# Performance work log

Measured on AMD Instinct MI355X. Metric: run time of the kernel, lower is better.

## Reference

```python
import jax, jax.numpy as jnp
import numpy as np

B, T = 1, 2048
N_HEAD = 16
N_KV_HEAD = 16
N_EMBD = 1024
HEAD_DIM = N_EMBD // N_HEAD  # 64
HD8 = HEAD_DIM // 8          # 8 octonion blocks per head
EPS_RMS = 1e-6


def qconj(q):
    return q * jnp.array([1.0, -1.0, -1.0, -1.0], dtype=q.dtype)


def qmul(q1, q2):
    # Hamilton product, (...,4) x (...,4) -> (...,4)
    w1, x1, y1, z1 = (q1[..., 0], q1[..., 1], q1[..., 2], q1[..., 3])
    w2, x2, y2, z2 = (q2[..., 0], q2[..., 1], q2[..., 2], q2[..., 3])
    return jnp.stack([
        w1 * w2 - x1 * x2 - y1 * y2 - z1 * z2,
        w1 * x2 + x1 * w2 + y1 * z2 - z1 * y2,
        w1 * y2 - x1 * z2 + y1 * w2 + z1 * x2,
        w1 * z2 + x1 * y2 - y1 * x2 + z1 * w2,
    ], axis=-1)


def omul(o1, o2):
    # Cayley-Dickson octonion product, (...,8)
    a, b = o1[..., :4], o1[..., 4:]
    c, d = o2[..., :4], o2[..., 4:]
    first = qmul(a, c) - qmul(qconj(d), b)
    second = qmul(d, a) + qmul(b, qconj(c))
    return jnp.concatenate([first, second], axis=-1)


def oconj(o):
    return jnp.concatenate([qconj(o[..., :4]), -o[..., 4:]], axis=-1)


# Octonion multiplication structure constants: omul(x, y)[k] = x[a] y[p] C[a,p,k]
_EYE8 = jnp.eye(8, dtype=jnp.float32)
C_OCT = jax.vmap(lambda ei: jax.vmap(lambda ej: omul(ei, ej))(_EYE8))(_EYE8)  # (8,8,8)
# Trilinear tensor for omul(omul(q, kc), v):  T3[a,p,q,k] = sum_e C[a,p,e] C[e,q,k]
T3 = jnp.einsum('ape,eqk->apqk', C_OCT, C_OCT)  # (8,8,8,8)


def apply_rotary_emb(x, cos, sin):
    # x: (B, T, H, hd); cos/sin: (1, T, 1, hd//2)
    d = x.shape[-1] // 2
    x1, x2 = x[..., :d], x[..., d:]
    y1 = x1 * cos + x2 * sin
    y2 = x2 * cos - x1 * sin
    return jnp.concatenate([y1, y2], axis=-1)


def rms_norm(x):
    return x * jax.lax.rsqrt(jnp.mean(x * x, axis=-1, keepdims=True) + EPS_RMS)


def setup_inputs() -> dict:
    key = jax.random.key(0)
    ks = jax.random.split(key, 7)
    x = jax.random.normal(ks[0], (B, T, N_EMBD), dtype=jnp.float32)
    cos = jax.random.uniform(ks[1], (1, T, 1, HEAD_DIM // 2), dtype=jnp.float32)
    sin = jax.random.uniform(ks[2], (1, T, 1, HEAD_DIM // 2), dtype=jnp.float32)
    s = 0.02
    Wq = jax.random.normal(ks[3], (N_HEAD * HEAD_DIM, N_EMBD), dtype=jnp.float32) * s
    Wk = jax.random.normal(ks[4], (N_KV_HEAD * HEAD_DIM, N_EMBD), dtype=jnp.float32) * s
    Wv = jax.random.normal(ks[5], (N_KV_HEAD * HEAD_DIM, N_EMBD), dtype=jnp.float32) * s
    Wo = jax.random.normal(ks[6], (N_EMBD, N_EMBD), dtype=jnp.float32) * s
    return {"x": x, "cos": cos, "sin": sin, "Wq": Wq, "Wk": Wk, "Wv": Wv, "Wo": Wo}


def reference(x, cos, sin, Wq, Wk, Wv, Wo):
    Bx, Tx, Cx = x.shape
    q = (x @ Wq.T).reshape(Bx, Tx, N_HEAD, HEAD_DIM)
    k = (x @ Wk.T).reshape(Bx, Tx, N_KV_HEAD, HEAD_DIM)
    v = (x @ Wv.T).reshape(Bx, Tx, N_KV_HEAD, HEAD_DIM)
    q = rms_norm(apply_rotary_emb(q, cos, sin))
    k = rms_norm(apply_rotary_emb(k, cos, sin))
    q = q.transpose(0, 2, 1, 3)  # (B,H,T,hd)
    k = k.transpose(0, 2, 1, 3)
    v = v.transpose(0, 2, 1, 3)

    q_o = q.reshape(Bx, N_HEAD, Tx, HD8, 8)
    k_o = k.reshape(Bx, N_KV_HEAD, Tx, HD8, 8)
    v_o = v.reshape(Bx, N_KV_HEAD, Tx, HD8, 8)
    # F.normalize(p=2, dim=-1): divide by max(||.||, 1e-12)
    k_o = k_o / jnp.maximum(jnp.linalg.norm(k_o, axis=-1, keepdims=True), 1e-12)

    # Scores use the (pre-octonion-normalized) rotary+rms k
    scores = jnp.einsum('bhid,bhjd->bhij', q, k) * (HEAD_DIM ** -0.5)
    mask = jnp.tril(jnp.ones((Tx, Tx), dtype=bool))
    scores = jnp.where(mask, scores, -jnp.inf)
    probs = jax.nn.softmax(scores, axis=-1)  # (B,H,Tq,Tk)

    # y_i = sum_j p_ij * omul(omul(q_i, oconj(k_j)), v_j)
    # omul is bilinear, so pull the j-sum inside:
    # y_i[k] = q_i[a] * T3[a,p,c,k] * (sum_j p_ij kc_j[p] v_j[c])
    kc = oconj(k_o)                                              # (B,H,Tk,M,8)
    KV = jnp.einsum('bhjmp,bhjmq->bhjmpq', kc, v_o)              # (B,H,Tk,M,8,8)
    Z = jnp.einsum('bhij,bhjmpq->bhimpq', probs, KV)             # (B,H,Tq,M,8,8)
    y_o = jnp.einsum('bhima,apqk,bhimpq->bhimk', q_o, T3, Z)     # (B,H,Tq,M,8)

    y = y_o.reshape(Bx, N_HEAD, Tx, HEAD_DIM).transpose(0, 2, 1, 3).reshape(Bx, Tx, Cx)
    return y @ Wo.T
```

## Files before the change

kernel.cpp:

```cpp
#include <hip/hip_runtime.h>

typedef unsigned short u16;
typedef unsigned int u32;

#define T_SEQ 2048
#define NHEAD 16
#define HDIM 64
#define CDIM 1024
#define W_HSTR (512*2048)
#define Z_HSTR (2048*512)

#define SGBITS 0xB2D8741EACC66A00ULL

#define EXP2C 0.18033688011112042f

typedef _Float16 f16x8 __attribute__((ext_vector_type(8)));
typedef float f32x4 __attribute__((ext_vector_type(4)));

__device__ __forceinline__ float h2f(u16 u) { _Float16 h; __builtin_memcpy(&h, &u, 2); return (float)h; }
__device__ __forceinline__ u16 f2h(float f) { _Float16 h = (_Float16)f; u16 u; __builtin_memcpy(&u, &h, 2); return u; }
__device__ __forceinline__ u32 pk(float a, float b) { return (u32)f2h(a) | ((u32)f2h(b) << 16); }

__device__ __forceinline__ void gload16(const u16* g, u16* l) {
    __builtin_amdgcn_global_load_lds((const __attribute__((address_space(1))) u32*)g,
                                     (__attribute__((address_space(3))) u32*)l, 16, 0, 0);
}

template<bool F16OUT>
__device__ __forceinline__ void hgemm_tile(const u16* __restrict__ At, int lda,
                                           const u16* __restrict__ Bt, int ldb, int K,
                                           float* __restrict__ Cf, u16* __restrict__ Ch,
                                           int ldc, float scale, u16* As, u16* Bs) {
    int t = threadIdx.x;
    int wave = t >> 6, l = t & 63;
    int wm = wave & 1, wn = wave >> 1;
    int quad = l >> 4, lr = l & 15;
    f32x4 acc[4][4];
#pragma unroll
    for (int i = 0; i < 4; ++i)
#pragma unroll
        for (int j = 0; j < 4; ++j) acc[i][j] = (f32x4){0.f, 0.f, 0.f, 0.f};
    int acol = quad * 8;
    for (int k0 = 0; k0 < K; k0 += 64) {
#pragma unroll
        for (int j = 0; j < 4; ++j) {
            int d = wave * 4 + j;
            int kb = d >> 3, seg = d & 7;
            size_t roff = (size_t)(seg * 16 + lr);
            int coff = k0 + kb * 32 + acol;
            gload16(At + roff * lda + coff, As + d * 512);
            gload16(Bt + roff * ldb + coff, Bs + d * 512);
        }
        __syncthreads();
#pragma unroll
        for (int kb = 0; kb < 2; ++kb) {
            f16x8 af[4], bf[4];
#pragma unroll
            for (int mi = 0; mi < 4; ++mi) af[mi] = *(const f16x8*)&As[(kb * 8 + wm * 4 + mi) * 512 + l * 8];
#pragma unroll
            for (int ni = 0; ni < 4; ++ni) bf[ni] = *(const f16x8*)&Bs[(kb * 8 + wn * 4 + ni) * 512 + l * 8];
#pragma unroll
            for (int mi = 0; mi < 4; ++mi)
#pragma unroll
                for (int ni = 0; ni < 4; ++ni)
                    acc[mi][ni] = __builtin_amdgcn_mfma_f32_16x16x32_f16(af[mi], bf[ni], acc[mi][ni], 0, 0, 0);
        }
        __syncthreads();
    }
#pragma unroll
    for (int mi = 0; mi < 4; ++mi)
#pragma unroll
        for (int ni = 0; ni < 4; ++ni)
#pragma unroll
            for (int rr = 0; rr < 4; ++rr) {
                int gr = wm * 64 + mi * 16 + quad * 4 + rr;
                int gc = wn * 64 + ni * 16 + lr;
                float v = acc[mi][ni][rr] * scale;
                if (F16OUT) Ch[(size_t)gr * ldc + gc] = f2h(v);
                else Cf[(size_t)gr * ldc + gc] = v;
            }
}

__global__ __launch_bounds__(256) void hgemm_f32(const u16* __restrict__ A, int lda,
                                                 const u16* __restrict__ B, int ldb,
                                                 float* __restrict__ C, int ldc, int K) {
    __shared__ u16 As[8192], Bs[8192];
    int bm = blockIdx.y * 128, bn = blockIdx.x * 128;
    hgemm_tile<false>(A + (size_t)bm * lda, lda, B + (size_t)bn * ldb, ldb, K,
                      C + (size_t)bm * ldc + bn, nullptr, ldc, 1.f, As, Bs);
}

__global__ __launch_bounds__(256) void hgemm_f16(const u16* __restrict__ A, int lda,
                                                 const u16* __restrict__ B, int ldb,
                                                 u16* __restrict__ C, int ldc, int K) {
    __shared__ u16 As[8192], Bs[8192];
    int bm = blockIdx.y * 128, bn = blockIdx.x * 128;
    hgemm_tile<true>(A + (size_t)bm * lda, lda, B + (size_t)bn * ldb, ldb, K,
                     nullptr, C + (size_t)bm * ldc + bn, ldc, 1.f, As, Bs);
}

__global__ __launch_bounds__(512, 4) void flash_pw(const u16* __restrict__ q16,
                                                   const u16* __restrict__ k16,
                                                   const u16* __restrict__ W,
                                                   u16* __restrict__ Z,
                                                   float* __restrict__ lbuf) {
    __shared__ u16 Pl[2][128 * 136];
    int idx = blockIdx.x;
    int pair = idx & 255, half = idx >> 8;
    int g = pair & 31;
    int rbh = pair >> 5;
    int rb = half ? rbh : 15 - rbh;
    int h = ((g & 7) << 1) | ((g >> 3) & 1);
    int nq2 = g >> 4;
    int t = threadIdx.x;
    int wave = t >> 6, l = t & 63;
    int wm = wave & 1, wn = wave >> 1;
    int quad = l >> 4, lr = l & 15;

    const u16* qbase = q16 + (size_t)(rb * 128 + wm * 64 + lr) * CDIM + h * HDIM + quad * 8;
    f16x8 qa[4][2];
#pragma unroll
    for (int mi = 0; mi < 4; ++mi)
#pragma unroll
        for (int kb = 0; kb < 2; ++kb)
            qa[mi][kb] = *(const f16x8*)(qbase + (size_t)(mi * 16) * CDIM + kb * 32);

    f32x4 accz[4][4];
    f32x4 accl[4];
#pragma unroll
    for (int mi = 0; mi < 4; ++mi) {
        accl[mi] = (f32x4){0.f, 0.f, 0.f, 0.f};
#pragma unroll
        for (int ni = 0; ni < 4; ++ni) accz[mi][ni] = (f32x4){0.f, 0.f, 0.f, 0.f};
    }
    f16x8 ones;
#pragma unroll
    for (int j = 0; j < 8; ++j) ones[j] = (_Float16)1.0f;

    const u16* kbase = k16 + (size_t)(wn * 32 + lr) * CDIM + h * HDIM + quad * 8;
    const u16* Wbase = W + (size_t)h * W_HSTR + (size_t)(nq2 * 256 + wn * 64 + lr) * T_SEQ + quad * 8;

    auto qk_expst = [&](int cb, u16* Pd) {
        f16x8 kf[2][2];
#pragma unroll
        for (int ni = 0; ni < 2; ++ni)
#pragma unroll
            for (int kb = 0; kb < 2; ++kb)
                kf[ni][kb] = *(const f16x8*)(kbase + (size_t)(cb * 128 + ni * 16) * CDIM + kb * 32);
#pragma unroll
        for (int mi = 0; mi < 4; ++mi) {
            int row = wm * 64 + mi * 16 + quad * 4;
#pragma unroll
            for (int ni = 0; ni < 2; ++ni) {
                f32x4 s = (f32x4){0.f, 0.f, 0.f, 0.f};
                s = __builtin_amdgcn_mfma_f32_16x16x32_f16(qa[mi][0], kf[ni][0], s, 0, 0, 0);
                s = __builtin_amdgcn_mfma_f32_16x16x32_f16(qa[mi][1], kf[ni][1], s, 0, 0, 0);
                int col = wn * 32 + ni * 16 + lr;
#pragma unroll
                for (int rr = 0; rr < 4; ++rr) {
                    bool valid = (cb < rb) | (col <= row + rr);
                    float p = valid ? __builtin_amdgcn_exp2f(s[rr] * EXP2C - 12.f) : 0.f;
                    Pd[(row + rr) * 136 + col] = f2h(p);
                }
            }
        }
    };
    auto pw = [&](int cb, const u16* Ps) {
#pragma unroll
        for (int kb = 0; kb < 4; ++kb) {
            f16x8 pf[4], wf[4];
#pragma unroll
            for (int ni = 0; ni < 4; ++ni)
                wf[ni] = *(const f16x8*)(Wbase + (size_t)(ni * 16) * T_SEQ + cb * 128 + kb * 32);
#pragma unroll
            for (int mi = 0; mi < 4; ++mi)
                pf[mi] = *(const f16x8*)&Ps[(wm * 64 + mi * 16 + lr) * 136 + kb * 32 + quad * 8];
#pragma unroll
            for (int mi = 0; mi < 4; ++mi)
#pragma unroll
                for (int ni = 0; ni < 4; ++ni)
                    accz[mi][ni] = __builtin_amdgcn_mfma_f32_16x16x32_f16(pf[mi], wf[ni], accz[mi][ni], 0, 0, 0);
            if (nq2 == 0 && wn == 0)
#pragma unroll
                for (int mi = 0; mi < 4; ++mi)
                    accl[mi] = __builtin_amdgcn_mfma_f32_16x16x32_f16(pf[mi], ones, accl[mi], 0, 0, 0);
        }
    };

    qk_expst(0, Pl[0]);
    int cur = 0;
    for (int cb = 1; cb <= rb; ++cb) {
        __syncthreads();
        qk_expst(cb, Pl[cur ^ 1]);
        pw(cb - 1, Pl[cur]);
        cur ^= 1;
    }
    __syncthreads();
    pw(rb, Pl[cur]);

    u16* Zb = Z + (size_t)h * Z_HSTR;
#pragma unroll
    for (int mi = 0; mi < 4; ++mi)
#pragma unroll
        for (int rr = 0; rr < 4; ++rr) {
            int row = rb * 128 + wm * 64 + mi * 16 + quad * 4 + rr;
#pragma unroll
            for (int ni = 0; ni < 4; ++ni) {
                int col = nq2 * 256 + wn * 64 + ni * 16 + lr;
                Zb[(size_t)row * 512 + col] = f2h(accz[mi][ni][rr]);
            }
        }
    if (nq2 == 0 && wn == 0 && lr == 0) {
#pragma unroll
        for (int mi = 0; mi < 4; ++mi) {
            int row = rb * 128 + wm * 64 + mi * 16 + quad * 4;
            *(f32x4*)(lbuf + h * T_SEQ + row) = accl[mi];
        }
    }
}

__global__ __launch_bounds__(256) void cvt5(const float* __restrict__ x, const float* __restrict__ wq,
                                            const float* __restrict__ wk, const float* __restrict__ wv,
                                            const float* __restrict__ wo,
                                            u16* __restrict__ x16, u16* __restrict__ w16) {
    int z = blockIdx.y;
    size_t base = ((size_t)blockIdx.x * 256 + threadIdx.x) * 8;
    const float* src;
    u16* dst;
    size_t cnt;
    if (z == 0) { src = x; dst = x16; cnt = 2097152; }
    else if (z == 1) { src = wq; dst = w16; cnt = 1048576; }
    else if (z == 2) { src = wk; dst = w16 + 1048576; cnt = 1048576; }
    else if (z == 3) { src = wv; dst = w16 + 2097152; cnt = 1048576; }
    else { src = wo; dst = w16 + 3145728; cnt = 1048576; }
    if (base >= cnt) return;
    float4 f0 = *(const float4*)(src + base);
    float4 f1 = *(const float4*)(src + base + 4);
    uint4 o;
    o.x = pk(f0.x, f0.y); o.y = pk(f0.z, f0.w); o.z = pk(f1.x, f1.y); o.w = pk(f1.z, f1.w);
    *(uint4*)(dst + base) = o;
}

__global__ __launch_bounds__(256) void prep_rope(const u16* __restrict__ qkv,
                                                 u16* __restrict__ q16, u16* __restrict__ k16,
                                                 float* __restrict__ kc,
                                                 const float* __restrict__ cosb, const float* __restrict__ sinb) {
    int wave = threadIdx.x >> 6, lane = threadIdx.x & 63;
    int idx = blockIdx.x * 4 + wave;
    int t = idx >> 4, h = idx & 15;
    int d = lane & 31;
    float cs = cosb[t * 32 + d];
    float sn = sinb[t * 32 + d];
    size_t b3 = (size_t)t * 3072 + h * HDIM;
    size_t b1 = (size_t)t * CDIM + h * HDIM;

    float xq = h2f(qkv[b3 + lane]);
    float oq = __shfl(xq, lane ^ 32);
    float rq = (lane < 32) ? fmaf(xq, cs, oq * sn) : fmaf(xq, cs, -oq * sn);
    float ssq = rq * rq;
#pragma unroll
    for (int m = 1; m < 64; m <<= 1) ssq += __shfl_xor(ssq, m);
    rq *= rsqrtf(ssq * (1.f / 64.f) + 1e-6f);
    q16[b1 + lane] = f2h(rq);

    float xk = h2f(qkv[b3 + 1024 + lane]);
    float ok = __shfl(xk, lane ^ 32);
    float rk = (lane < 32) ? fmaf(xk, cs, ok * sn) : fmaf(xk, cs, -ok * sn);
    float ssk = rk * rk;
#pragma unroll
    for (int m = 1; m < 64; m <<= 1) ssk += __shfl_xor(ssk, m);
    rk *= rsqrtf(ssk * (1.f / 64.f) + 1e-6f);
    k16[b1 + lane] = f2h(rk);

    float s8 = rk * rk;
    s8 += __shfl_xor(s8, 1); s8 += __shfl_xor(s8, 2); s8 += __shfl_xor(s8, 4);
    float sc2 = 1.f / fmaxf(sqrtf(s8), 1e-12f);
    float kcv = rk * sc2;
    if (lane & 7) kcv = -kcv;
    kc[b1 + lane] = kcv;
}

__global__ __launch_bounds__(256) void w_pre(const float* __restrict__ kc, const u16* __restrict__ qkv,
                                             u16* __restrict__ W) {
    __shared__ float kcs[64][65];
    __shared__ float vs[64][65];
    int h = blockIdx.y;
    int j0 = blockIdx.x * 64;
    int t = threadIdx.x;
    int r = t >> 2, cq = (t & 3) * 16;
    const float* kp = kc + (size_t)(j0 + r) * CDIM + h * HDIM + cq;
    const u16* vp = qkv + (size_t)(j0 + r) * 3072 + 2048 + h * HDIM + cq;
#pragma unroll
    for (int u4 = 0; u4 < 4; ++u4) {
        float4 a = *(const float4*)(kp + u4 * 4);
        ushort4 b = *(const ushort4*)(vp + u4 * 4);
        kcs[r][cq + u4 * 4 + 0] = a.x; kcs[r][cq + u4 * 4 + 1] = a.y;
        kcs[r][cq + u4 * 4 + 2] = a.z; kcs[r][cq + u4 * 4 + 3] = a.w;
        vs[r][cq + u4 * 4 + 0] = h2f(b.x); vs[r][cq + u4 * 4 + 1] = h2f(b.y);
        vs[r][cq + u4 * 4 + 2] = h2f(b.z); vs[r][cq + u4 * 4 + 3] = h2f(b.w);
    }
    __syncthreads();
    int j = t & 63, g = t >> 6;
    u16* Wp = W + (size_t)h * W_HSTR + j0 + j;
    for (int ae = g * 16; ae < g * 16 + 16; ++ae) {
        int a = ae >> 3, e = ae & 7;
        u32 mask = 0;
#pragma unroll
        for (int qq = 0; qq < 8; ++qq) {
            int p = a ^ e ^ qq;
            u32 bit = (u32)(((SGBITS >> (a * 8 + p)) ^ (SGBITS >> ((e ^ qq) * 8 + qq))) & 1ULL);
            mask |= bit << qq;
        }
#pragma unroll
        for (int m = 0; m < 8; ++m) {
            float w = 0.f;
#pragma unroll
            for (int qq = 0; qq < 8; ++qq) {
                float t1 = kcs[j][m * 8 + (a ^ e ^ qq)] * vs[j][m * 8 + qq];
                w = ((mask >> qq) & 1) ? (w - t1) : (w + t1);
            }
            Wp[(size_t)(m * 64 + ae) * T_SEQ] = f2h(w);
        }
    }
}

__global__ __launch_bounds__(256) void contract_y(const u16* __restrict__ q16, const u16* __restrict__ Z,
                                                  const float* __restrict__ lbuf, u16* __restrict__ y16) {
    __shared__ u16 zb[4][512];
    int wave = threadIdx.x >> 6, lane = threadIdx.x & 63;
    int idx = blockIdx.x * 4 + wave;
    int i = idx >> 4, h = idx & 15;
    uint4 zv = *(const uint4*)(Z + (size_t)h * Z_HSTR + (size_t)i * 512 + lane * 8);
    *(uint4*)&zb[wave][lane * 8] = zv;
    int m = lane >> 3, e = lane & 7;
    const u16* qp = q16 + (size_t)i * CDIM + h * HDIM + m * 8;
    uint4 qb = *(const uint4*)qp;
    float qv[8];
    qv[0] = h2f(qb.x & 0xffff); qv[1] = h2f(qb.x >> 16);
    qv[2] = h2f(qb.y & 0xffff); qv[3] = h2f(qb.y >> 16);
    qv[4] = h2f(qb.z & 0xffff); qv[5] = h2f(qb.z >> 16);
    qv[6] = h2f(qb.w & 0xffff); qv[7] = h2f(qb.w >> 16);
    float linv = 1.f / lbuf[h * T_SEQ + i];
    __syncthreads();
    float acc = 0.f;
#pragma unroll
    for (int a = 0; a < 8; ++a) acc = fmaf(qv[a], h2f(zb[wave][m * 64 + a * 8 + e]), acc);
    y16[(size_t)i * CDIM + h * HDIM + lane] = f2h(acc * linv);
}

extern "C" void kernel_launch(void* const* d_in, const int* in_sizes, int n_in,
                              void* d_out, int out_size, void* d_ws, size_t ws_size,
                              hipStream_t stream) {
    const float* x = (const float*)d_in[0];
    const float* cosb = (const float*)d_in[1];
    const float* sinb = (const float*)d_in[2];
    const float* Wq = (const float*)d_in[3];
    const float* Wk = (const float*)d_in[4];
    const float* Wv = (const float*)d_in[5];
    const float* Wo = (const float*)d_in[6];
    float* out = (float*)d_out;
    char* base = (char*)d_ws;
    u16* qkv16 = (u16*)base;
    float* kc = (float*)(base + 12582912);
    u16* x16 = (u16*)(base + 20971520);
    u16* w16 = (u16*)(base + 25165824);
    u16* q16 = (u16*)(base + 33554432);
    u16* k16 = (u16*)(base + 37748736);
    u16* y16 = (u16*)(base + 41943040);
    u16* W = (u16*)(base + 46137344);
    u16* Z = (u16*)(base + 79691776);
    float* lbuf = (float*)(base + 113246208);

    cvt5<<<dim3(1024, 5), 256, 0, stream>>>(x, Wq, Wk, Wv, Wo, x16, w16);
    hgemm_f16<<<dim3(24, 16), 256, 0, stream>>>(x16, CDIM, w16, CDIM, qkv16, 3072, CDIM);
    prep_rope<<<T_SEQ * NHEAD / 4, 256, 0, stream>>>(qkv16, q16, k16, kc, cosb, sinb);
    w_pre<<<dim3(32, 16), 256, 0, stream>>>(kc, qkv16, W);
    flash_pw<<<512, 512, 0, stream>>>(q16, k16, W, Z, lbuf);
    contract_y<<<NHEAD * T_SEQ / 4, 256, 0, stream>>>(q16, Z, lbuf, y16);
    hgemm_f32<<<dim3(8, 16), 256, 0, stream>>>(y16, CDIM, w16 + 3145728, CDIM, out, CDIM, CDIM);
}
```

Measured before the change: 329.8 us.

## Split flash_pw query blocks to 64 rows with 4-wave blocks and balanced scheduling

Shrinks each flash_pw block from 128 query rows over 8 waves to 64 query rows over 4 waves, so twice as many blocks are launched. The key loop still steps in 128-wide chunks, and the causal mask now uses absolute row and column positions. Query blocks are mapped to four slots that pair short and long causal rows to balance load. This aims to cut tail imbalance and raise occupancy, but each block reloads the W and K tiles for half as many rows, so global traffic per unit of work roughly doubles.

```diff
diff --git a/kernel.cpp b/kernel.cpp
--- a/kernel.cpp
+++ b/kernel.cpp
@@ -99,25 +99,32 @@
                      nullptr, C + (size_t)bm * ldc + bn, ldc, 1.f, As, Bs);
 }
 
-__global__ __launch_bounds__(512, 4) void flash_pw(const u16* __restrict__ q16,
+__global__ __launch_bounds__(256, 4) void flash_pw(const u16* __restrict__ q16,
                                                    const u16* __restrict__ k16,
                                                    const u16* __restrict__ W,
                                                    u16* __restrict__ Z,
                                                    float* __restrict__ lbuf) {
-    __shared__ u16 Pl[2][128 * 136];
+    __shared__ u16 Pl[2][64 * 136];
     int idx = blockIdx.x;
-    int pair = idx & 255, half = idx >> 8;
-    int g = pair & 31;
-    int rbh = pair >> 5;
-    int rb = half ? rbh : 15 - rbh;
+    int slot = idx >> 8;
+    int low = idx & 255;
+    int rbp = low >> 5;
+    int g = low & 31;
     int h = ((g & 7) << 1) | ((g >> 3) & 1);
     int nq2 = g >> 4;
+    int rb;
+    if (slot == 0) rb = rbp;
+    else if (slot == 1) rb = 31 - rbp;
+    else if (slot == 2) rb = 8 + rbp;
+    else rb = 23 - rbp;
+    int cb_last = rb >> 1;
+    int row0 = rb * 64;
     int t = threadIdx.x;
     int wave = t >> 6, l = t & 63;
-    int wm = wave & 1, wn = wave >> 1;
+    int wn = wave;
     int quad = l >> 4, lr = l & 15;
 
-    const u16* qbase = q16 + (size_t)(rb * 128 + wm * 64 + lr) * CDIM + h * HDIM + quad * 8;
+    const u16* qbase = q16 + (size_t)(row0 + lr) * CDIM + h * HDIM + quad * 8;
     f16x8 qa[4][2];
 #pragma unroll
     for (int mi = 0; mi < 4; ++mi)
@@ -149,7 +156,7 @@
                 kf[ni][kb] = *(const f16x8*)(kbase + (size_t)(cb * 128 + ni * 16) * CDIM + kb * 32);
 #pragma unroll
         for (int mi = 0; mi < 4; ++mi) {
-            int row = wm * 64 + mi * 16 + quad * 4;
+            int row = mi * 16 + quad * 4;
 #pragma unroll
             for (int ni = 0; ni < 2; ++ni) {
                 f32x4 s = (f32x4){0.f, 0.f, 0.f, 0.f};
@@ -158,7 +165,7 @@
                 int col = wn * 32 + ni * 16 + lr;
 #pragma unroll
                 for (int rr = 0; rr < 4; ++rr) {
-                    bool valid = (cb < rb) | (col <= row + rr);
+                    bool valid = (cb < cb_last) | (cb * 128 + col <= row0 + row + rr);
                     float p = valid ? __builtin_amdgcn_exp2f(s[rr] * EXP2C - 12.f) : 0.f;
                     Pd[(row + rr) * 136 + col] = f2h(p);
                 }
@@ -174,7 +181,7 @@
                 wf[ni] = *(const f16x8*)(Wbase + (size_t)(ni * 16) * T_SEQ + cb * 128 + kb * 32);
 #pragma unroll
             for (int mi = 0; mi < 4; ++mi)
-                pf[mi] = *(const f16x8*)&Ps[(wm * 64 + mi * 16 + lr) * 136 + kb * 32 + quad * 8];
+                pf[mi] = *(const f16x8*)&Ps[(mi * 16 + lr) * 136 + kb * 32 + quad * 8];
 #pragma unroll
             for (int mi = 0; mi < 4; ++mi)
 #pragma unroll
@@ -189,21 +196,21 @@
 
     qk_expst(0, Pl[0]);
     int cur = 0;
-    for (int cb = 1; cb <= rb; ++cb) {
+    for (int cb = 1; cb <= cb_last; ++cb) {
         __syncthreads();
         qk_expst(cb, Pl[cur ^ 1]);
         pw(cb - 1, Pl[cur]);
         cur ^= 1;
     }
     __syncthreads();
-    pw(rb, Pl[cur]);
+    pw(cb_last, Pl[cur]);
 
     u16* Zb = Z + (size_t)h * Z_HSTR;
 #pragma unroll
     for (int mi = 0; mi < 4; ++mi)
 #pragma unroll
         for (int rr = 0; rr < 4; ++rr) {
-            int row = rb * 128 + wm * 64 + mi * 16 + quad * 4 + rr;
+            int row = row0 + mi * 16 + quad * 4 + rr;
 #pragma unroll
             for (int ni = 0; ni < 4; ++ni) {
                 int col = nq2 * 256 + wn * 64 + ni * 16 + lr;
@@ -213,7 +220,7 @@
     if (nq2 == 0 && wn == 0 && lr == 0) {
 #pragma unroll
         for (int mi = 0; mi < 4; ++mi) {
-            int row = rb * 128 + wm * 64 + mi * 16 + quad * 4;
+            int row = row0 + mi * 16 + quad * 4;
             *(f32x4*)(lbuf + h * T_SEQ + row) = accl[mi];
         }
     }
@@ -375,7 +382,7 @@
     hgemm_f16<<<dim3(24, 16), 256, 0, stream>>>(x16, CDIM, w16, CDIM, qkv16, 3072, CDIM);
     prep_rope<<<T_SEQ * NHEAD / 4, 256, 0, stream>>>(qkv16, q16, k16, kc, cosb, sinb);
     w_pre<<<dim3(32, 16), 256, 0, stream>>>(kc, qkv16, W);
-    flash_pw<<<512, 512, 0, stream>>>(q16, k16, W, Z, lbuf);
+    flash_pw<<<1024, 256, 0, stream>>>(q16, k16, W, Z, lbuf);
     contract_y<<<NHEAD * T_SEQ / 4, 256, 0, stream>>>(q16, Z, lbuf, y16);
     hgemm_f32<<<dim3(8, 16), 256, 0, stream>>>(y16, CDIM, w16 + 3145728, CDIM, out, CDIM, CDIM);
 }
```

New measurement: 377.7 us. 14.5% more time.
